# Performance work log

Hardware: AMD Instinct MI355X
Metric: run time of the kernel (lower is better)

The kernel has to match this reference:

```python
import jax, jax.numpy as jnp
import numpy as np


def setup_inputs() -> dict:
    key = jax.random.key(0)
    B, C, H, W = 8, 512, 64, 64
    x = jax.random.normal(key, (B, C, H, W), dtype=jnp.float32)
    # flag: 1 = masked (hole) position, 0 = known. Center-square hole as in
    # mask to this resolution; with shift_sz=1, mask_thred=1 flag == mask).
    flag = np.zeros((H, W), dtype=np.int32)
    flag[H // 4: 3 * H // 4, W // 4: 3 * W // 4] = 1
    return {"input": x, "flag": jnp.asarray(flag)}


def reference(input, flag):
    B, C, H, W = input.shape
    c2 = C // 2
    hw = H * W
    former = input[:, :c2]          # decoder features (B, c2, H, W)
    latter = input[:, c2:]          # encoder features (B, c2, H, W)

    ff = former.reshape(B, c2, hw)  # (B, c2, P)
    lf = latter.reshape(B, c2, hw)  # (B, c2, P)

    # L2-normalize latter pixel features (shift_sz=1 patches == pixels);
    # matches util.cosine_similarity's normalized conv kernels.
    norms = jnp.linalg.norm(lf, axis=1, keepdims=True)
    lnorm = lf / jnp.maximum(norms, 1e-8)

    # cosine[b, p, q] = <former[b,:,p], normed_latter[b,:,q]> for all positions;
    # masked q are excluded from the argmax (equiv. to gathering only the
    # non-mask patches via nonmask_point_idx, but jit-friendly fixed shapes).
    cos = jnp.einsum('bcp,bcq->bpq', ff, lnorm)
    flag_f = flag.reshape(hw)
    neg_inf = jnp.asarray(-jnp.inf, cos.dtype)
    cos = jnp.where(flag_f[None, None, :] == 1, neg_inf, cos)

    idx = jnp.argmax(cos, axis=2)   # (B, P): best non-mask source per position

    # Gather RAW latter features at best-match positions (util.shift_offsets
    # applies the 0/1 transition matrix ind_lst to the un-normalized latter).
    gidx = jnp.broadcast_to(idx[:, None, :], (B, c2, hw))
    shift = jnp.take_along_axis(lf, gidx, axis=2)            # (B, c2, P)
    shift = jnp.where(flag_f[None, None, :] == 1, shift, 0.0)  # zeros at known px
    shift = shift.reshape(B, c2, H, W)

    return jnp.concatenate([former, latter, shift], axis=1)   # (B, 3*c2, H, W)
```

## Files before the change

### kernel.cpp

```cpp
#include <hip/hip_runtime.h>
#include <stdint.h>
#include <math.h>

#define HW   4096
#define NB   8
#define NC   512
#define C2   256
#define PT   32
#define QC   384
#define NCHK 11

#define WS_PACKED 0
#define WS_Q0     393216
#define WS_P1     409600
#define WS_CNT    425984
#define WS_INVC   558080

__device__ __forceinline__ unsigned long long mkkey(float v, unsigned q) {
    unsigned u = __float_as_uint(v);
    u = (u & 0x80000000u) ? ~u : (u | 0x80000000u);
    return ((unsigned long long)u << 32) | (unsigned long long)(0xFFFFFFFFu - q);
}

__device__ __forceinline__ float* lfc_region(float* out, int b) {
    return out + ((size_t)b * 768 + 512) * HW;
}

__global__ void compact_kernel(const int* __restrict__ flag, int* __restrict__ q0,
                               int* __restrict__ p1, int* __restrict__ cnt) {
    __shared__ int c1s[256];
    int t = threadIdx.x;
    int f[16]; int n1 = 0;
    #pragma unroll
    for (int j = 0; j < 16; ++j) { f[j] = flag[t*16 + j]; n1 += (f[j] == 1); }
    c1s[t] = n1;
    __syncthreads();
    if (t == 0) {
        int run = 0;
        for (int i = 0; i < 256; ++i) { int v = c1s[i]; c1s[i] = run; run += v; }
        cnt[0] = run;
        cnt[1] = HW - run;
    }
    __syncthreads();
    int b1 = c1s[t];
    int b0 = t*16 - c1s[t];
    for (int j = 0; j < 16; ++j) {
        int i = t*16 + j;
        if (f[j] == 1) p1[b1++] = i; else q0[b0++] = i;
    }
}

__global__ void pack_kernel(const float* __restrict__ x,
                            const int* __restrict__ q0, const int* __restrict__ p1,
                            const int* __restrict__ cnt, float* __restrict__ out) {
    int b = blockIdx.z, cy = blockIdx.y;
    int n1 = cnt[0], n0 = cnt[1];
    int ns = (n0 + 3) & ~3, ms = (n1 + 3) & ~3;
    int i = blockIdx.x * 256 + threadIdx.x;
    if (cy < C2) {
        if (i >= n0) return;
        float* lfc = lfc_region(out, b);
        lfc[(size_t)cy * ns + i] = x[((size_t)b * NC + C2 + cy) * HW + q0[i]];
    } else {
        int c = cy - C2;
        if (i >= n1) return;
        float* ffc = lfc_region(out, b) + (size_t)C2 * ns;
        ffc[(size_t)c * ms + i] = x[((size_t)b * NC + c) * HW + p1[i]];
    }
}

__global__ void invc_kernel(const float* __restrict__ out, const int* __restrict__ cnt,
                            float* __restrict__ invc) {
    int b = blockIdx.y;
    int n0 = cnt[1];
    int ns = (n0 + 3) & ~3;
    int k = blockIdx.x * 256 + threadIdx.x;
    if (k >= n0) return;
    const float* lfc = lfc_region((float*)out, b) + k;
    float s = 0.f;
    #pragma unroll 8
    for (int c = 0; c < C2; ++c) {
        float v = lfc[(size_t)c * ns];
        s = fmaf(v, v, s);
    }
    invc[b * HW + k] = 1.0f / fmaxf(sqrtf(s), 1e-8f);
}

__global__ void __launch_bounds__(256) argmax_kernel(
        float* __restrict__ out, const float* __restrict__ invc,
        const int* __restrict__ q0, const int* __restrict__ p1,
        const int* __restrict__ cnt, unsigned long long* __restrict__ packed) {
    int bid   = blockIdx.x;
    int b     = bid & 7;
    int s     = bid >> 3;
    int chunk = s >> 5;
    int tile  = s & 31;
    int n1 = cnt[0], n0 = cnt[1];
    if (tile * PT >= n1) return;
    if (chunk * QC >= n0) return;
    int ns = (n0 + 3) & ~3, ms = (n1 + 3) & ~3;

    __shared__ float sff[128][PT];

    int t = threadIdx.x;
    int tp = t >> 6;
    int tq = t & 63;

    const float* lfc = lfc_region(out, b);
    const float* ffc = lfc + (size_t)C2 * ns;
    int kbase = chunk * QC + tq * 6;

    const float* r = lfc + kbase;
    float2 b0 = *(const float2*)(r);
    float2 b1 = *(const float2*)(r + 2);
    float2 b2 = *(const float2*)(r + 4);

    float acc[8][6];
    #pragma unroll
    for (int pi = 0; pi < 8; ++pi)
        #pragma unroll
        for (int j = 0; j < 6; ++j) acc[pi][j] = 0.f;

    bool fulltile = (tile * PT + PT <= n1);

    for (int h = 0; h < 2; ++h) {
        __syncthreads();
        if (fulltile) {
            #pragma unroll
            for (int k = 0; k < 4; ++k) {
                int i4 = t + (k << 8);
                int c = i4 >> 3, jg = i4 & 7;
                ((float4*)sff)[i4] =
                    *(const float4*)&ffc[(size_t)(h * 128 + c) * ms + tile * PT + jg * 4];
            }
        } else {
            #pragma unroll
            for (int k = 0; k < 4; ++k) {
                int i4 = t + (k << 8);
                int c = i4 >> 3, jg = i4 & 7;
                const float* src = &ffc[(size_t)(h * 128 + c) * ms];
                int m0 = tile * PT + jg * 4;
                float4 v;
                v.x = (m0 + 0 < n1) ? src[m0 + 0] : 0.f;
                v.y = (m0 + 1 < n1) ? src[m0 + 1] : 0.f;
                v.z = (m0 + 2 < n1) ? src[m0 + 2] : 0.f;
                v.w = (m0 + 3 < n1) ? src[m0 + 3] : 0.f;
                ((float4*)sff)[i4] = v;
            }
        }
        __syncthreads();

        #pragma unroll 2
        for (int cc = 0; cc < 128; ++cc) {
            const float* prow = r + ns;
            float2 n0v = *(const float2*)(prow);
            float2 n1v = *(const float2*)(prow + 2);
            float2 n2v = *(const float2*)(prow + 4);
            const float4* arow = (const float4*)&sff[cc][tp * 8];
            float4 a0 = arow[0], a1 = arow[1];
            float av[8] = {a0.x, a0.y, a0.z, a0.w, a1.x, a1.y, a1.z, a1.w};
            float bvv[6] = {b0.x, b0.y, b1.x, b1.y, b2.x, b2.y};
            #pragma unroll
            for (int pi = 0; pi < 8; ++pi)
                #pragma unroll
                for (int j = 0; j < 6; ++j)
                    acc[pi][j] = fmaf(av[pi], bvv[j], acc[pi][j]);
            b0 = n0v; b1 = n1v; b2 = n2v;
            r = prow;
        }
    }

    float best[8];
    int   bq[8];
    #pragma unroll
    for (int pi = 0; pi < 8; ++pi) { best[pi] = -INFINITY; bq[pi] = 0x7FFFFFFF; }

    #pragma unroll
    for (int j = 0; j < 6; ++j) {
        int k = kbase + j;
        if (k >= n0) continue;
        float sc = invc[b * HW + k];
        int   q  = q0[k];
        #pragma unroll
        for (int pi = 0; pi < 8; ++pi) {
            float cv = acc[pi][j] * sc;
            if (cv > best[pi] || (cv == best[pi] && q < bq[pi])) {
                best[pi] = cv; bq[pi] = q;
            }
        }
    }

    #pragma unroll
    for (int m = 1; m < 64; m <<= 1) {
        #pragma unroll
        for (int pi = 0; pi < 8; ++pi) {
            float ov = __shfl_xor(best[pi], m);
            int   oq = __shfl_xor(bq[pi], m);
            if (ov > best[pi] || (ov == best[pi] && oq < bq[pi])) {
                best[pi] = ov; bq[pi] = oq;
            }
        }
    }
    if (tq == 0) {
        #pragma unroll
        for (int pi = 0; pi < 8; ++pi) {
            int pidx = tile * PT + tp * 8 + pi;
            int p = (pidx < n1) ? p1[pidx] : -1;
            if (p >= 0)
                atomicMax(&packed[(size_t)b * HW + p], mkkey(best[pi], (unsigned)bq[pi]));
        }
    }
}

__global__ void copy_kernel(const float4* __restrict__ x4, float4* __restrict__ out4) {
    size_t i = (size_t)blockIdx.x * 256 + threadIdx.x;
    if (i >= (size_t)NB * NC * (HW / 4)) return;
    size_t p4 = i & 1023;
    size_t c  = (i >> 10) & 511;
    size_t b  = i >> 19;
    out4[(b * 768 + c) * 1024 + p4] = x4[i];
}

__global__ void shift_kernel(const float* __restrict__ x, const int* __restrict__ flag,
                             const unsigned long long* __restrict__ packed,
                             float* __restrict__ out) {
    int cc = blockIdx.x, b = blockIdx.y;
    const float* lfrow = x + ((size_t)b * NC + C2 + cc) * HW;
    float*       orow  = out + ((size_t)b * 768 + 512 + cc) * HW;
    const unsigned long long* pk = packed + (size_t)b * HW;
    for (int p = threadIdx.x; p < HW; p += 256) {
        float v = 0.f;
        if (flag[p] == 1) {
            unsigned low = (unsigned)(pk[p] & 0xFFFFFFFFull);
            int q = (int)((0xFFFFFFFFu - low) & (HW - 1));
            v = lfrow[q];
        }
        orow[p] = v;
    }
}

extern "C" void kernel_launch(void* const* d_in, const int* in_sizes, int n_in,
                              void* d_out, int out_size, void* d_ws, size_t ws_size,
                              hipStream_t stream) {
    const float* x    = (const float*)d_in[0];
    const int*   flag = (const int*)d_in[1];
    float*       out  = (float*)d_out;
    char*        ws   = (char*)d_ws;

    unsigned long long* packed = (unsigned long long*)(ws + WS_PACKED);
    int*   q0   = (int*)(ws + WS_Q0);
    int*   p1   = (int*)(ws + WS_P1);
    int*   cnt  = (int*)(ws + WS_CNT);
    float* invc = (float*)(ws + WS_INVC);

    hipMemsetAsync(packed, 0, (size_t)NB * HW * sizeof(unsigned long long), stream);

    compact_kernel<<<1, 256, 0, stream>>>(flag, q0, p1, cnt);
    pack_kernel<<<dim3(HW / 256, NC, NB), 256, 0, stream>>>(x, q0, p1, cnt, out);
    invc_kernel<<<dim3(HW / 256, NB), 256, 0, stream>>>(out, cnt, invc);
    copy_kernel<<<(NB * NC * (HW / 4) + 255) / 256, 256, 0, stream>>>((const float4*)x, (float4*)out);
    argmax_kernel<<<dim3(NB * NCHK * 32), 256, 0, stream>>>(out, invc, q0, p1, cnt, packed);
    shift_kernel<<<dim3(C2, NB), 256, 0, stream>>>(x, flag, packed, out);
}
```

Measured before the change: 274.1 us.

## Fuse input copy into pack kernel and retile argmax to float4 columns

The separate copy kernel is removed; the pack kernel now copies each input row to the output while also gathering the compacted former/latter columns from the same row, so the input is read once. The argmax kernel switches from 6 columns per thread loaded as three float2 to 4 columns per thread loaded as one float4. The chunk size drops from 384 to 256 (16 chunks), and the k loop is unrolled by two with prefetch. This trades fewer accumulators per thread and more blocks for wider vector loads, and avoids one full pass over the input.

```diff
diff --git a/kernel.cpp b/kernel.cpp
--- a/kernel.cpp
+++ b/kernel.cpp
@@ -7,8 +7,8 @@
 #define NC   512
 #define C2   256
 #define PT   32
-#define QC   384
-#define NCHK 11
+#define QC   256
+#define NCHK 16
 
 #define WS_PACKED 0
 #define WS_Q0     393216
@@ -54,18 +54,22 @@
                             const int* __restrict__ q0, const int* __restrict__ p1,
                             const int* __restrict__ cnt, float* __restrict__ out) {
     int b = blockIdx.z, cy = blockIdx.y;
+    int i = blockIdx.x * 256 + threadIdx.x;
     int n1 = cnt[0], n0 = cnt[1];
     int ns = (n0 + 3) & ~3, ms = (n1 + 3) & ~3;
-    int i = blockIdx.x * 256 + threadIdx.x;
+    const float* xrow = x + ((size_t)b * NC + cy) * HW;
+    out[((size_t)b * 768 + cy) * HW + i] = xrow[i];
     if (cy < C2) {
-        if (i >= n0) return;
-        float* lfc = lfc_region(out, b);
-        lfc[(size_t)cy * ns + i] = x[((size_t)b * NC + C2 + cy) * HW + q0[i]];
+        if (i < n1) {
+            float* ffc = lfc_region(out, b) + (size_t)C2 * ns;
+            ffc[(size_t)cy * ms + i] = xrow[p1[i]];
+        }
     } else {
         int c = cy - C2;
-        if (i >= n1) return;
-        float* ffc = lfc_region(out, b) + (size_t)C2 * ns;
-        ffc[(size_t)c * ms + i] = x[((size_t)b * NC + c) * HW + p1[i]];
+        if (i < n0) {
+            float* lfc = lfc_region(out, b);
+            lfc[(size_t)c * ns + i] = xrow[q0[i]];
+        }
     }
 }
 
@@ -108,18 +112,17 @@
 
     const float* lfc = lfc_region(out, b);
     const float* ffc = lfc + (size_t)C2 * ns;
-    int kbase = chunk * QC + tq * 6;
+    int kbase = chunk * QC + tq * 4;
 
     const float* r = lfc + kbase;
-    float2 b0 = *(const float2*)(r);
-    float2 b1 = *(const float2*)(r + 2);
-    float2 b2 = *(const float2*)(r + 4);
-
-    float acc[8][6];
+    float4 f0 = *(const float4*)(r);
+    float4 f1 = *(const float4*)(r + ns);
+
+    float acc[8][4];
     #pragma unroll
     for (int pi = 0; pi < 8; ++pi)
         #pragma unroll
-        for (int j = 0; j < 6; ++j) acc[pi][j] = 0.f;
+        for (int j = 0; j < 4; ++j) acc[pi][j] = 0.f;
 
     bool fulltile = (tile * PT + PT <= n1);
 
@@ -151,22 +154,35 @@
         __syncthreads();
 
         #pragma unroll 2
-        for (int cc = 0; cc < 128; ++cc) {
-            const float* prow = r + ns;
-            float2 n0v = *(const float2*)(prow);
-            float2 n1v = *(const float2*)(prow + 2);
-            float2 n2v = *(const float2*)(prow + 4);
-            const float4* arow = (const float4*)&sff[cc][tp * 8];
-            float4 a0 = arow[0], a1 = arow[1];
-            float av[8] = {a0.x, a0.y, a0.z, a0.w, a1.x, a1.y, a1.z, a1.w};
-            float bvv[6] = {b0.x, b0.y, b1.x, b1.y, b2.x, b2.y};
-            #pragma unroll
-            for (int pi = 0; pi < 8; ++pi)
+        for (int cc = 0; cc < 128; cc += 2) {
+            float4 f2 = *(const float4*)(r + 2 * (size_t)ns);
+            {
+                const float4* arow = (const float4*)&sff[cc][tp * 8];
+                float4 a0 = arow[0], a1 = arow[1];
+                float av[8] = {a0.x, a0.y, a0.z, a0.w, a1.x, a1.y, a1.z, a1.w};
                 #pragma unroll
-                for (int j = 0; j < 6; ++j)
-                    acc[pi][j] = fmaf(av[pi], bvv[j], acc[pi][j]);
-            b0 = n0v; b1 = n1v; b2 = n2v;
-            r = prow;
+                for (int pi = 0; pi < 8; ++pi) {
+                    acc[pi][0] = fmaf(av[pi], f0.x, acc[pi][0]);
+                    acc[pi][1] = fmaf(av[pi], f0.y, acc[pi][1]);
+                    acc[pi][2] = fmaf(av[pi], f0.z, acc[pi][2]);
+                    acc[pi][3] = fmaf(av[pi], f0.w, acc[pi][3]);
+                }
+            }
+            float4 f3 = *(const float4*)(r + 3 * (size_t)ns);
+            {
+                const float4* arow = (const float4*)&sff[cc + 1][tp * 8];
+                float4 a0 = arow[0], a1 = arow[1];
+                float av[8] = {a0.x, a0.y, a0.z, a0.w, a1.x, a1.y, a1.z, a1.w};
+                #pragma unroll
+                for (int pi = 0; pi < 8; ++pi) {
+                    acc[pi][0] = fmaf(av[pi], f1.x, acc[pi][0]);
+                    acc[pi][1] = fmaf(av[pi], f1.y, acc[pi][1]);
+                    acc[pi][2] = fmaf(av[pi], f1.z, acc[pi][2]);
+                    acc[pi][3] = fmaf(av[pi], f1.w, acc[pi][3]);
+                }
+            }
+            f0 = f2; f1 = f3;
+            r += 2 * (size_t)ns;
         }
     }
 
@@ -176,7 +192,7 @@
     for (int pi = 0; pi < 8; ++pi) { best[pi] = -INFINITY; bq[pi] = 0x7FFFFFFF; }
 
     #pragma unroll
-    for (int j = 0; j < 6; ++j) {
+    for (int j = 0; j < 4; ++j) {
         int k = kbase + j;
         if (k >= n0) continue;
         float sc = invc[b * HW + k];
@@ -210,15 +226,6 @@
                 atomicMax(&packed[(size_t)b * HW + p], mkkey(best[pi], (unsigned)bq[pi]));
         }
     }
-}
-
-__global__ void copy_kernel(const float4* __restrict__ x4, float4* __restrict__ out4) {
-    size_t i = (size_t)blockIdx.x * 256 + threadIdx.x;
-    if (i >= (size_t)NB * NC * (HW / 4)) return;
-    size_t p4 = i & 1023;
-    size_t c  = (i >> 10) & 511;
-    size_t b  = i >> 19;
-    out4[(b * 768 + c) * 1024 + p4] = x4[i];
 }
 
 __global__ void shift_kernel(const float* __restrict__ x, const int* __restrict__ flag,
@@ -258,7 +265,6 @@
     compact_kernel<<<1, 256, 0, stream>>>(flag, q0, p1, cnt);
     pack_kernel<<<dim3(HW / 256, NC, NB), 256, 0, stream>>>(x, q0, p1, cnt, out);
     invc_kernel<<<dim3(HW / 256, NB), 256, 0, stream>>>(out, cnt, invc);
-    copy_kernel<<<(NB * NC * (HW / 4) + 255) / 256, 256, 0, stream>>>((const float4*)x, (float4*)out);
     argmax_kernel<<<dim3(NB * NCHK * 32), 256, 0, stream>>>(out, invc, q0, p1, cnt, packed);
     shift_kernel<<<dim3(C2, NB), 256, 0, stream>>>(x, flag, packed, out);
 }
```

Result: faster. 264.1 us (-3.7%).
